# Performance work log

Hardware: AMD Instinct MI355X
Metric: run time of the kernel (lower is better)

Reference implementation:

```python
import jax, jax.numpy as jnp
import numpy as np

EMBED_DIM = 1024
NUM_HEADS = 16
HEAD_DIM = EMBED_DIM // NUM_HEADS
SCALE = HEAD_DIM ** -0.5


def setup_inputs() -> dict:
    key = jax.random.key(0)
    ks = jax.random.split(key, 5)
    B, S = 4, 2048
    x = jax.random.normal(ks[0], (B, S, EMBED_DIM), dtype=jnp.float32)
    # Dense(embed_dim*3): kernel [D, 3D], bias [3D] (Keras glorot_uniform; use scaled normal)
    w_qkv = jax.random.normal(ks[1], (EMBED_DIM, 3 * EMBED_DIM), dtype=jnp.float32) * (1.0 / np.sqrt(EMBED_DIM))
    b_qkv = jnp.zeros((3 * EMBED_DIM,), dtype=jnp.float32)
    w_proj = jax.random.normal(ks[2], (EMBED_DIM, EMBED_DIM), dtype=jnp.float32) * (1.0 / np.sqrt(EMBED_DIM))
    b_proj = jnp.zeros((EMBED_DIM,), dtype=jnp.float32)
    return {"x": x, "w_qkv": w_qkv, "b_qkv": b_qkv, "w_proj": w_proj, "b_proj": b_proj}


def reference(x, w_qkv, b_qkv, w_proj, b_proj):
    B, S, D = x.shape
    qkv = x @ w_qkv + b_qkv
    qkv = qkv.reshape(B, S, 3, NUM_HEADS, HEAD_DIM)
    qkv = jnp.transpose(qkv, (2, 0, 3, 1, 4))
    q, k, v = qkv[0], qkv[1], qkv[2]
    # scaled dot-product attention (full [B,H,S,S] scores, matching source)
    attn_logits = jnp.einsum('bhqd,bhkd->bhqk', q, k) * SCALE
    attn = jax.nn.softmax(attn_logits, axis=-1)
    context = jnp.einsum('bhqk,bhkd->bhqd', attn, v)
    context = jnp.transpose(context, (0, 2, 1, 3)).reshape(B, S, D)
    out = context @ w_proj + b_proj
    return out
```

## Files before the change

### kernel.cpp

```cpp
#include <hip/hip_runtime.h>

typedef unsigned short u16;
typedef __attribute__((ext_vector_type(8))) short bf16x8;
typedef __attribute__((ext_vector_type(4))) float f32x4;
typedef __attribute__((ext_vector_type(16))) float f32x16;

__device__ __forceinline__ float bf2f(u16 x) {
  union { unsigned u; float f; } v; v.u = ((unsigned)x) << 16; return v.f;
}
__device__ __forceinline__ u16 f2bf(float f) {
  union { float f; unsigned u; } v; v.f = f;
  unsigned r = v.u + 0x7FFFu + ((v.u >> 16) & 1u);
  return (u16)(r >> 16);
}
__device__ __forceinline__ float clampf(float v) {
  return fmaxf(fminf(v, 1.0e4f), -1.0e4f);
}
__device__ __forceinline__ void gll16(const u16* g, u16* l) {
  __builtin_amdgcn_global_load_lds(
      (const __attribute__((address_space(1))) void*)g,
      (__attribute__((address_space(3))) void*)l, 16, 0, 0);
}
__device__ __forceinline__ unsigned cvtpk(float lo, float hi) {
  unsigned r;
  asm("v_cvt_pk_bf16_f32 %0, %1, %2" : "=v"(r) : "v"(lo), "v"(hi));
  return r;
}

__global__ __launch_bounds__(256) void fused_prep(
    const float* __restrict__ x,  u16* __restrict__ xbf,
    const float* __restrict__ wq, u16* __restrict__ wT1,
    const float* __restrict__ wp, u16* __restrict__ wT2) {
  __shared__ u16 tile[32][33];
  const int blk = blockIdx.x;
  if (blk < 8192) {
    const int i0 = (blk * 256 + threadIdx.x) * 4;
    const float4 v = *(const float4*)(x + i0);
    xbf[i0 + 0] = f2bf(v.x); xbf[i0 + 1] = f2bf(v.y);
    xbf[i0 + 2] = f2bf(v.z); xbf[i0 + 3] = f2bf(v.w);
    return;
  }
  const float* in; u16* outp; int R, C, bc, br;
  if (blk < 8192 + 3072) {
    const int u = blk - 8192;
    in = wq; outp = wT1; R = 1024; C = 3072;
    bc = (u % 96) * 32; br = (u / 96) * 32;
  } else {
    const int u = blk - 11264;
    in = wp; outp = wT2; R = 1024; C = 1024;
    bc = (u % 32) * 32; br = (u / 32) * 32;
  }
  const int tx = threadIdx.x & 31, ty = threadIdx.x >> 5;
  #pragma unroll
  for (int i = ty; i < 32; i += 8)
    tile[i][tx] = f2bf(in[(size_t)(br + i) * C + bc + tx]);
  __syncthreads();
  #pragma unroll
  for (int i = ty; i < 32; i += 8)
    outp[(size_t)(bc + i) * R + br + tx] = tile[tx][i];
}

__global__ __launch_bounds__(256) void gemm1_qkv(
    const u16* __restrict__ A, const u16* __restrict__ Bt,
    const float* __restrict__ bias, u16* __restrict__ qk,
    u16* __restrict__ vt, int K) {
  __shared__ u16 As0[128 * 32], As1[128 * 32];
  __shared__ u16 Bs0[128 * 32], Bs1[128 * 32];
  const int tid = threadIdx.x;
  const int m0 = blockIdx.x * 128, n0 = blockIdx.y * 128;
  const int wave = tid >> 6, lane = tid & 63;
  const int quad = lane >> 4, l16 = lane & 15;
  const int wm = (wave >> 1) * 64, wn = (wave & 1) * 64;
  const int sr = (lane >> 2), sp = lane & 3;

  f32x4 acc[4][4] = {};
  const u16* gA = A + (size_t)(m0 + wave * 32 + sr) * K + sp * 8;
  const u16* gB = Bt + (size_t)(n0 + wave * 32 + sr) * K + sp * 8;

  for (int k0 = 0; k0 < K; k0 += 64) {
    #pragma unroll
    for (int t = 0; t < 2; ++t) {
      gll16(gA + (size_t)(t * 16) * K + k0,      &As0[(wave * 32 + t * 16) * 32]);
      gll16(gA + (size_t)(t * 16) * K + k0 + 32, &As1[(wave * 32 + t * 16) * 32]);
      gll16(gB + (size_t)(t * 16) * K + k0,      &Bs0[(wave * 32 + t * 16) * 32]);
      gll16(gB + (size_t)(t * 16) * K + k0 + 32, &Bs1[(wave * 32 + t * 16) * 32]);
    }
    __syncthreads();
    #pragma unroll
    for (int ks = 0; ks < 2; ++ks) {
      const u16* Ah = ks ? As1 : As0;
      const u16* Bh = ks ? Bs1 : Bs0;
      bf16x8 af[4], bfr[4];
      #pragma unroll
      for (int i = 0; i < 4; ++i)
        af[i] = *(const bf16x8*)&Ah[(wm + i * 16 + l16) * 32 + quad * 8];
      #pragma unroll
      for (int j = 0; j < 4; ++j)
        bfr[j] = *(const bf16x8*)&Bh[(wn + j * 16 + l16) * 32 + quad * 8];
      #pragma unroll
      for (int i = 0; i < 4; ++i)
        #pragma unroll
        for (int j = 0; j < 4; ++j)
          acc[i][j] = __builtin_amdgcn_mfma_f32_16x16x32_bf16(af[i], bfr[j], acc[i][j], 0, 0, 0);
    }
    __syncthreads();
  }

  const float c2q = 0.125f * 1.44269504088896340736f;
  #pragma unroll
  for (int i = 0; i < 4; ++i) {
    const int row = m0 + wm + i * 16 + quad * 4;
    #pragma unroll
    for (int j = 0; j < 4; ++j) {
      const int col = n0 + wn + j * 16 + l16;
      const float bv = bias[col];
      if (col < 1024) {
        #pragma unroll
        for (int r = 0; r < 4; ++r)
          qk[(size_t)(row + r) * 2048 + col] = f2bf(clampf(acc[i][j][r] + bv) * c2q);
      } else if (col < 2048) {
        #pragma unroll
        for (int r = 0; r < 4; ++r)
          qk[(size_t)(row + r) * 2048 + col] = f2bf(clampf(acc[i][j][r] + bv));
      } else {
        const int d = col & 63;
        const int hh = (col - 2048) >> 6;
        #pragma unroll
        for (int r = 0; r < 4; ++r) {
          const int rr = row + r;
          const int bb = rr >> 11, ss = rr & 2047;
          vt[(size_t)(bb * 16 + hh) * 131072 + d * 2048 + ss] =
              f2bf(clampf(acc[i][j][r] + bv));
        }
      }
    }
  }
}

__global__ __launch_bounds__(256) void gemm2_proj(
    const u16* __restrict__ A, const u16* __restrict__ Bt,
    const float* __restrict__ bias, float* __restrict__ out, int K) {
  __shared__ u16 As0[64 * 32], As1[64 * 32];
  __shared__ u16 Bs0[128 * 32], Bs1[128 * 32];
  const int tid = threadIdx.x;
  const int m0 = blockIdx.x * 64, n0 = blockIdx.y * 128;
  const int wave = tid >> 6, lane = tid & 63;
  const int quad = lane >> 4, l16 = lane & 15;
  const int wm = (wave >> 1) * 32, wn = (wave & 1) * 64;
  const int sr = (lane >> 2), sp = lane & 3;

  f32x4 acc[2][4] = {};
  const u16* gA = A + (size_t)(m0 + wave * 16 + sr) * K + sp * 8;
  const u16* gB = Bt + (size_t)(n0 + wave * 32 + sr) * K + sp * 8;

  for (int k0 = 0; k0 < K; k0 += 64) {
    gll16(gA + k0,      &As0[(wave * 16) * 32]);
    gll16(gA + k0 + 32, &As1[(wave * 16) * 32]);
    #pragma unroll
    for (int t = 0; t < 2; ++t) {
      gll16(gB + (size_t)(t * 16) * K + k0,      &Bs0[(wave * 32 + t * 16) * 32]);
      gll16(gB + (size_t)(t * 16) * K + k0 + 32, &Bs1[(wave * 32 + t * 16) * 32]);
    }
    __syncthreads();
    #pragma unroll
    for (int ks = 0; ks < 2; ++ks) {
      const u16* Ah = ks ? As1 : As0;
      const u16* Bh = ks ? Bs1 : Bs0;
      bf16x8 af[2], bfr[4];
      #pragma unroll
      for (int i = 0; i < 2; ++i)
        af[i] = *(const bf16x8*)&Ah[(wm + i * 16 + l16) * 32 + quad * 8];
      #pragma unroll
      for (int j = 0; j < 4; ++j)
        bfr[j] = *(const bf16x8*)&Bh[(wn + j * 16 + l16) * 32 + quad * 8];
      #pragma unroll
      for (int i = 0; i < 2; ++i)
        #pragma unroll
        for (int j = 0; j < 4; ++j)
          acc[i][j] = __builtin_amdgcn_mfma_f32_16x16x32_bf16(af[i], bfr[j], acc[i][j], 0, 0, 0);
    }
    __syncthreads();
  }

  #pragma unroll
  for (int i = 0; i < 2; ++i) {
    const int row = m0 + wm + i * 16 + quad * 4;
    #pragma unroll
    for (int j = 0; j < 4; ++j) {
      const int col = n0 + wn + j * 16 + l16;
      const float bv = bias[col];
      #pragma unroll
      for (int r = 0; r < 4; ++r)
        out[(size_t)(row + r) * 1024 + col] = clampf(acc[i][j][r] + bv);
    }
  }
}

__device__ __forceinline__ int swz(int row, int col) {
  const int key = (row ^ (row >> 2)) & 7;
  return row * 64 + (((col >> 3) ^ key) << 3) + (col & 7);
}

__global__ __launch_bounds__(256, 4) void attn_fused(
    const u16* __restrict__ qk, const u16* __restrict__ vt,
    u16* __restrict__ ctx) {
  __shared__ u16 Ks[64 * 64];
  __shared__ u16 VsT[64 * 64];
  const int bh = blockIdx.x, qt = blockIdx.y;
  const int b = bh >> 4, h = bh & 15;
  const int tid = threadIdx.x;
  const int w = tid >> 6, lane = tid & 63;
  const int l31 = lane & 31, hl = lane >> 5;
  const int qbase = qt * 128 + w * 32;

  const u16* qptr = qk + (size_t)(b * 2048) * 2048 + h * 64;
  bf16x8 qf[4];
  #pragma unroll
  for (int ds = 0; ds < 4; ++ds)
    qf[ds] = *(const bf16x8*)(qptr + (size_t)(qbase + l31) * 2048 + ds * 16 + hl * 8);

  const u16* kptr = qk + (size_t)(b * 2048) * 2048 + 1024 + h * 64;
  const u16* vptr = vt + (size_t)bh * 131072;

  const int srow = tid >> 3, scol = (tid & 7) * 8;

  const int st0 = swz(srow, scol);
  const int st1 = swz(srow + 32, scol);
  int off[2][4];
  #pragma unroll
  for (int a = 0; a < 2; ++a)
    #pragma unroll
    for (int d = 0; d < 4; ++d)
      off[a][d] = swz(a * 32 + l31, d * 16 + hl * 8);

  const u16* kB0 = kptr + (size_t)srow * 2048 + scol;
  const u16* kB1 = kptr + (size_t)(srow + 32) * 2048 + scol;
  const u16* vB0 = vptr + (size_t)srow * 2048 + scol;
  const u16* vB1 = vptr + (size_t)(srow + 32) * 2048 + scol;

  f32x16 o[2] = {};
  f32x16 lsum = {};
  const f32x16 fz = {};
  const short one = (short)0x3F80;
  const bf16x8 ones = {one, one, one, one, one, one, one, one};

  bf16x8 k0 = *(const bf16x8*)kB0;
  bf16x8 k1 = *(const bf16x8*)kB1;
  bf16x8 v0 = *(const bf16x8*)vB0;
  bf16x8 v1 = *(const bf16x8*)vB1;

  for (int kv0 = 0; kv0 < 2048; kv0 += 64) {
    __syncthreads();
    *(bf16x8*)&Ks[st0]  = k0;
    *(bf16x8*)&Ks[st1]  = k1;
    *(bf16x8*)&VsT[st0] = v0;
    *(bf16x8*)&VsT[st1] = v1;
    __syncthreads();
    const int kvn = (kv0 + 64) & 2047;
    k0 = *(const bf16x8*)(kB0 + (size_t)kvn * 2048);
    k1 = *(const bf16x8*)(kB1 + (size_t)kvn * 2048);
    v0 = *(const bf16x8*)(vB0 + kvn);
    v1 = *(const bf16x8*)(vB1 + kvn);

    #pragma unroll
    for (int kb = 0; kb < 2; ++kb) {
      f32x16 s;
      __builtin_amdgcn_s_setprio(1);
      {
        bf16x8 kf = *(const bf16x8*)&Ks[off[kb][0]];
        s = __builtin_amdgcn_mfma_f32_32x32x16_bf16(kf, qf[0], fz, 0, 0, 0);
      }
      #pragma unroll
      for (int ds = 1; ds < 4; ++ds) {
        bf16x8 kf = *(const bf16x8*)&Ks[off[kb][ds]];
        s = __builtin_amdgcn_mfma_f32_32x32x16_bf16(kf, qf[ds], s, 0, 0, 0);
      }
      __builtin_amdgcn_s_setprio(0);
      #pragma unroll
      for (int r = 0; r < 16; ++r)
        s[r] = __builtin_amdgcn_exp2f(s[r]);
      #pragma unroll
      for (int ksl = 0; ksl < 2; ++ksl) {
        const int r0 = ksl * 8;
        unsigned cA = cvtpk(s[r0 + 0], s[r0 + 1]);
        unsigned cB = cvtpk(s[r0 + 2], s[r0 + 3]);
        unsigned cC = cvtpk(s[r0 + 4], s[r0 + 5]);
        unsigned cD = cvtpk(s[r0 + 6], s[r0 + 7]);
        asm volatile("v_permlane32_swap_b32 %0, %1" : "+v"(cA), "+v"(cC));
        asm volatile("v_permlane32_swap_b32 %0, %1" : "+v"(cB), "+v"(cD));
        union { unsigned u[4]; bf16x8 v; } pf;
        pf.u[0] = cA;
        pf.u[1] = cB;
        pf.u[2] = cC;
        pf.u[3] = cD;
        const int kg = kb * 2 + ksl;
        __builtin_amdgcn_s_setprio(1);
        lsum = __builtin_amdgcn_mfma_f32_32x32x16_bf16(pf.v, ones, lsum, 0, 0, 0);
        #pragma unroll
        for (int db = 0; db < 2; ++db) {
          bf16x8 vf = *(const bf16x8*)&VsT[off[db][kg]];
          o[db] = __builtin_amdgcn_mfma_f32_32x32x16_bf16(pf.v, vf, o[db], 0, 0, 0);
        }
        __builtin_amdgcn_s_setprio(0);
      }
    }
  }

  u16* cbase = ctx + (size_t)(b * 2048) * 1024 + h * 64;
  #pragma unroll
  for (int r = 0; r < 16; ++r) {
    const int q0 = (r & 3) + 8 * (r >> 2) + 4 * hl;
    const float inv = 1.0f / lsum[r];
    const size_t qrow = (size_t)(qbase + q0);
    cbase[qrow * 1024 + l31]      = f2bf(o[0][r] * inv);
    cbase[qrow * 1024 + 32 + l31] = f2bf(o[1][r] * inv);
  }
}

extern "C" void kernel_launch(void* const* d_in, const int* in_sizes, int n_in,
                              void* d_out, int out_size, void* d_ws, size_t ws_size,
                              hipStream_t stream) {
  (void)out_size;
  const float *x = nullptr, *wq = nullptr, *bq = nullptr, *wp = nullptr, *bp = nullptr;
  for (int i = 0; i < n_in; ++i) {
    switch (in_sizes[i]) {
      case 8388608: x  = (const float*)d_in[i]; break;
      case 3145728: wq = (const float*)d_in[i]; break;
      case 3072:    bq = (const float*)d_in[i]; break;
      case 1048576: wp = (const float*)d_in[i]; break;
      case 1024:    bp = (const float*)d_in[i]; break;
      default: break;
    }
  }
  if (!x || !wq || !bq || !wp || !bp) {
    x  = (const float*)d_in[0]; wq = (const float*)d_in[1];
    bq = (const float*)d_in[2]; wp = (const float*)d_in[3];
    bp = (const float*)d_in[4];
  }
  float* out = (float*)d_out;

  const size_t NEED = 75497472;
  if (ws_size < NEED) return;

  char* ws = (char*)d_ws;
  u16* qkb = (u16*)(ws);
  u16* vt  = (u16*)(ws + 33554432);
  u16* xbf = (u16*)(ws + 50331648);
  u16* wT1 = (u16*)(ws + 67108864);
  u16* wT2 = (u16*)(ws + 73400320);

  fused_prep<<<12288, 256, 0, stream>>>(x, xbf, wq, wT1, wp, wT2);
  gemm1_qkv<<<dim3(64, 24), 256, 0, stream>>>(xbf, wT1, bq, qkb, vt, 1024);
  attn_fused<<<dim3(64, 16), 256, 0, stream>>>(qkb, vt, xbf );
  gemm2_proj<<<dim3(128, 8), 256, 0, stream>>>(xbf , wT2, bp, out, 1024);
}
```

Measured before the change: 276.1 us.

## Swizzle QKV GEMM block order, transpose MFMA for V stores, vectorize bf16 cast

```diff
diff --git a/kernel.cpp b/kernel.cpp
--- a/kernel.cpp
+++ b/kernel.cpp
@@ -36,8 +36,9 @@
   if (blk < 8192) {
     const int i0 = (blk * 256 + threadIdx.x) * 4;
     const float4 v = *(const float4*)(x + i0);
-    xbf[i0 + 0] = f2bf(v.x); xbf[i0 + 1] = f2bf(v.y);
-    xbf[i0 + 2] = f2bf(v.z); xbf[i0 + 3] = f2bf(v.w);
+    ushort4 sv;
+    sv.x = f2bf(v.x); sv.y = f2bf(v.y); sv.z = f2bf(v.z); sv.w = f2bf(v.w);
+    *(ushort4*)(xbf + i0) = sv;
     return;
   }
   const float* in; u16* outp; int R, C, bc, br;
@@ -67,7 +68,9 @@
   __shared__ u16 As0[128 * 32], As1[128 * 32];
   __shared__ u16 Bs0[128 * 32], Bs1[128 * 32];
   const int tid = threadIdx.x;
-  const int m0 = blockIdx.x * 128, n0 = blockIdx.y * 128;
+  const int id = blockIdx.y * 64 + blockIdx.x;
+  const int sid = (id & 7) * 192 + (id >> 3);
+  const int m0 = (sid & 63) * 128, n0 = (sid >> 6) * 128;
   const int wave = tid >> 6, lane = tid & 63;
   const int quad = lane >> 4, l16 = lane & 15;
   const int wm = (wave >> 1) * 64, wn = (wave & 1) * 64;
@@ -77,60 +80,99 @@
   const u16* gA = A + (size_t)(m0 + wave * 32 + sr) * K + sp * 8;
   const u16* gB = Bt + (size_t)(n0 + wave * 32 + sr) * K + sp * 8;
 
-  for (int k0 = 0; k0 < K; k0 += 64) {
-    #pragma unroll
-    for (int t = 0; t < 2; ++t) {
-      gll16(gA + (size_t)(t * 16) * K + k0,      &As0[(wave * 32 + t * 16) * 32]);
-      gll16(gA + (size_t)(t * 16) * K + k0 + 32, &As1[(wave * 32 + t * 16) * 32]);
-      gll16(gB + (size_t)(t * 16) * K + k0,      &Bs0[(wave * 32 + t * 16) * 32]);
-      gll16(gB + (size_t)(t * 16) * K + k0 + 32, &Bs1[(wave * 32 + t * 16) * 32]);
-    }
-    __syncthreads();
-    #pragma unroll
-    for (int ks = 0; ks < 2; ++ks) {
-      const u16* Ah = ks ? As1 : As0;
-      const u16* Bh = ks ? Bs1 : Bs0;
-      bf16x8 af[4], bfr[4];
-      #pragma unroll
-      for (int i = 0; i < 4; ++i)
-        af[i] = *(const bf16x8*)&Ah[(wm + i * 16 + l16) * 32 + quad * 8];
-      #pragma unroll
-      for (int j = 0; j < 4; ++j)
-        bfr[j] = *(const bf16x8*)&Bh[(wn + j * 16 + l16) * 32 + quad * 8];
-      #pragma unroll
-      for (int i = 0; i < 4; ++i)
+  if (n0 < 2048) {
+    for (int k0 = 0; k0 < K; k0 += 64) {
+      #pragma unroll
+      for (int t = 0; t < 2; ++t) {
+        gll16(gA + (size_t)(t * 16) * K + k0,      &As0[(wave * 32 + t * 16) * 32]);
+        gll16(gA + (size_t)(t * 16) * K + k0 + 32, &As1[(wave * 32 + t * 16) * 32]);
+        gll16(gB + (size_t)(t * 16) * K + k0,      &Bs0[(wave * 32 + t * 16) * 32]);
+        gll16(gB + (size_t)(t * 16) * K + k0 + 32, &Bs1[(wave * 32 + t * 16) * 32]);
+      }
+      __syncthreads();
+      #pragma unroll
+      for (int ks = 0; ks < 2; ++ks) {
+        const u16* Ah = ks ? As1 : As0;
+        const u16* Bh = ks ? Bs1 : Bs0;
+        bf16x8 af[4], bfr[4];
+        #pragma unroll
+        for (int i = 0; i < 4; ++i)
+          af[i] = *(const bf16x8*)&Ah[(wm + i * 16 + l16) * 32 + quad * 8];
         #pragma unroll
         for (int j = 0; j < 4; ++j)
-          acc[i][j] = __builtin_amdgcn_mfma_f32_16x16x32_bf16(af[i], bfr[j], acc[i][j], 0, 0, 0);
-    }
-    __syncthreads();
-  }
-
-  const float c2q = 0.125f * 1.44269504088896340736f;
-  #pragma unroll
-  for (int i = 0; i < 4; ++i) {
-    const int row = m0 + wm + i * 16 + quad * 4;
+          bfr[j] = *(const bf16x8*)&Bh[(wn + j * 16 + l16) * 32 + quad * 8];
+        #pragma unroll
+        for (int i = 0; i < 4; ++i)
+          #pragma unroll
+          for (int j = 0; j < 4; ++j)
+            acc[i][j] = __builtin_amdgcn_mfma_f32_16x16x32_bf16(af[i], bfr[j], acc[i][j], 0, 0, 0);
+      }
+      __syncthreads();
+    }
+
+    const float c2q = 0.125f * 1.44269504088896340736f;
+    #pragma unroll
+    for (int i = 0; i < 4; ++i) {
+      const int row = m0 + wm + i * 16 + quad * 4;
+      #pragma unroll
+      for (int j = 0; j < 4; ++j) {
+        const int col = n0 + wn + j * 16 + l16;
+        const float bv = bias[col];
+        if (col < 1024) {
+          #pragma unroll
+          for (int r = 0; r < 4; ++r)
+            qk[(size_t)(row + r) * 2048 + col] = f2bf(clampf(acc[i][j][r] + bv) * c2q);
+        } else {
+          #pragma unroll
+          for (int r = 0; r < 4; ++r)
+            qk[(size_t)(row + r) * 2048 + col] = f2bf(clampf(acc[i][j][r] + bv));
+        }
+      }
+    }
+  } else {
+    for (int k0 = 0; k0 < K; k0 += 64) {
+      #pragma unroll
+      for (int t = 0; t < 2; ++t) {
+        gll16(gA + (size_t)(t * 16) * K + k0,      &As0[(wave * 32 + t * 16) * 32]);
+        gll16(gA + (size_t)(t * 16) * K + k0 + 32, &As1[(wave * 32 + t * 16) * 32]);
+        gll16(gB + (size_t)(t * 16) * K + k0,      &Bs0[(wave * 32 + t * 16) * 32]);
+        gll16(gB + (size_t)(t * 16) * K + k0 + 32, &Bs1[(wave * 32 + t * 16) * 32]);
+      }
+      __syncthreads();
+      #pragma unroll
+      for (int ks = 0; ks < 2; ++ks) {
+        const u16* Ah = ks ? As1 : As0;
+        const u16* Bh = ks ? Bs1 : Bs0;
+        bf16x8 af[4], bfr[4];
+        #pragma unroll
+        for (int i = 0; i < 4; ++i)
+          af[i] = *(const bf16x8*)&Ah[(wm + i * 16 + l16) * 32 + quad * 8];
+        #pragma unroll
+        for (int j = 0; j < 4; ++j)
+          bfr[j] = *(const bf16x8*)&Bh[(wn + j * 16 + l16) * 32 + quad * 8];
+        #pragma unroll
+        for (int i = 0; i < 4; ++i)
+          #pragma unroll
+          for (int j = 0; j < 4; ++j)
+            acc[i][j] = __builtin_amdgcn_mfma_f32_16x16x32_bf16(bfr[j], af[i], acc[i][j], 0, 0, 0);
+      }
+      __syncthreads();
+    }
+
     #pragma unroll
     for (int j = 0; j < 4; ++j) {
-      const int col = n0 + wn + j * 16 + l16;
-      const float bv = bias[col];
-      if (col < 1024) {
-        #pragma unroll
-        for (int r = 0; r < 4; ++r)
-          qk[(size_t)(row + r) * 2048 + col] = f2bf(clampf(acc[i][j][r] + bv) * c2q);
-      } else if (col < 2048) {
-        #pragma unroll
-        for (int r = 0; r < 4; ++r)
-          qk[(size_t)(row + r) * 2048 + col] = f2bf(clampf(acc[i][j][r] + bv));
-      } else {
-        const int d = col & 63;
-        const int hh = (col - 2048) >> 6;
+      const int cnb = n0 + wn + j * 16 + quad * 4;
+      const float4 bv4 = *(const float4*)&bias[cnb];
+      #pragma unroll
+      for (int i = 0; i < 4; ++i) {
+        const int cm = m0 + wm + i * 16 + l16;
+        const int bb = cm >> 11, ss = cm & 2047;
         #pragma unroll
         for (int r = 0; r < 4; ++r) {
-          const int rr = row + r;
-          const int bb = rr >> 11, ss = rr & 2047;
+          const int cn = cnb + r;
+          const int d = cn & 63, hh = (cn - 2048) >> 6;
           vt[(size_t)(bb * 16 + hh) * 131072 + d * 2048 + ss] =
-              f2bf(clampf(acc[i][j][r] + bv));
+              f2bf(clampf(acc[i][j][r] + ((const float*)&bv4)[r]));
         }
       }
     }
```

After: 281.3 us. About the same (+1.9%).
